# Performance work log

Measured on AMD Instinct MI355X. Metric: run time of the kernel, lower is better.

## Reference

```python
import jax, jax.numpy as jnp
import numpy as np

DIM = 1536
NH = 12
HD = DIM // NH          # 128
C = HD // 2             # 64 complex freq slots per head
DT = C - 2 * (C // 3)   # 22 temporal
DS = C // 3             # 21 per spatial axis
EPS = 1e-6
M_TAB = 64              # rope table length (>= max(f,h,w))


def _rope_tables():
    def tab(d):
        inv = 1.0 / (10000.0 ** (np.arange(d, dtype=np.float64) / d))
        ang = np.outer(np.arange(M_TAB, dtype=np.float64), inv)
        return np.cos(ang), np.sin(ang)
    ct, st = tab(DT)
    ch, sh = tab(DS)
    cw, sw = tab(DS)
    fc = np.concatenate([ct, ch, cw], axis=1).astype(np.float32)  # [M, 64]
    fs = np.concatenate([st, sh, sw], axis=1).astype(np.float32)
    return jnp.asarray(fc), jnp.asarray(fs)


def setup_inputs() -> dict:
    key = jax.random.key(0)
    ks = jax.random.split(key, 6)
    B, F, H, W = 1, 8, 22, 40
    L = F * H * W  # 7040
    s = 0.02
    x = jax.random.normal(ks[0], (B, L, DIM), jnp.float32)
    Wq = jax.random.normal(ks[1], (DIM, DIM), jnp.float32) * s
    Wk = jax.random.normal(ks[2], (DIM, DIM), jnp.float32) * s
    Wv = jax.random.normal(ks[3], (DIM, DIM), jnp.float32) * s
    Wo = jax.random.normal(ks[4], (DIM, DIM), jnp.float32) * s
    bk2 = jax.random.split(ks[5], 4)
    bq = jax.random.normal(bk2[0], (DIM,), jnp.float32) * s
    bk = jax.random.normal(bk2[1], (DIM,), jnp.float32) * s
    bv = jax.random.normal(bk2[2], (DIM,), jnp.float32) * s
    bo = jax.random.normal(bk2[3], (DIM,), jnp.float32) * s
    fc, fs = _rope_tables()
    return dict(x=x, Wq=Wq, bq=bq, Wk=Wk, bk=bk, Wv=Wv, bv=bv, Wo=Wo, bo=bo,
                gq=jnp.ones((DIM,), jnp.float32), gk=jnp.ones((DIM,), jnp.float32),
                freqs_cos=fc, freqs_sin=fs,
                num_frames=F, grid_h=H, grid_w=W,
                chunk_size=2, sink_size=1, max_attention_size=2640)


def _pos_table(tab, f, h, w):
    # tab: [M, 64] -> per-token [f*h*w, 64] via (t,h,w) axis split [22,21,21]
    t = jnp.broadcast_to(tab[:f, :DT][:, None, None, :], (f, h, w, DT))
    hh = jnp.broadcast_to(tab[:h, DT:DT + DS][None, :, None, :], (f, h, w, DS))
    ww = jnp.broadcast_to(tab[:w, DT + DS:][None, None, :, :], (f, h, w, DS))
    return jnp.concatenate([t, hh, ww], axis=-1).reshape(f * h * w, C)


def _forward(x, Wq, bq, Wk, bk, Wv, bv, Wo, bo, gq, gk, freqs_cos, freqs_sin,
             num_frames, grid_h, grid_w, chunk_size, sink_size, max_attention_size):
    B, L, D = x.shape
    lin = lambda t, W, b: jnp.einsum('bld,ed->ble', t, W) + b
    rms = lambda t, g: t * jax.lax.rsqrt(jnp.mean(t * t, axis=-1, keepdims=True) + EPS) * g

    q = rms(lin(x, Wq, bq), gq).reshape(B, L, NH, HD)
    k = rms(lin(x, Wk, bk), gk).reshape(B, L, NH, HD)
    v = lin(x, Wv, bv).reshape(B, L, NH, HD)

    # causal RoPE (start_frame=0)
    cosL = _pos_table(freqs_cos, num_frames, grid_h, grid_w)  # [L, 64]
    sinL = _pos_table(freqs_sin, num_frames, grid_h, grid_w)

    def rope(t):
        a = t.reshape(B, L, NH, C, 2)
        xr, xi = a[..., 0], a[..., 1]
        co = cosL[None, :, None, :]
        si = sinL[None, :, None, :]
        return jnp.stack([xr * co - xi * si, xr * si + xi * co], axis=-1).reshape(B, L, NH, HD)

    q = rope(q)
    k = rope(k)

    # loop attention, diffusion forcing: chunk i attends [0,(i+1)*block) with sink+window
    frame_seqlen = grid_h * grid_w
    block = frame_seqlen * chunk_size
    total_len = num_frames * frame_seqlen
    sink_end = sink_size * frame_seqlen
    num_chunks = -(-total_len // block)
    scale = 1.0 / (HD ** 0.5)

    def attn(qi, ki, vi):
        s = jnp.einsum('bqnd,bknd->bnqk', qi, ki) * scale
        p = jax.nn.softmax(s, axis=-1)
        return jnp.einsum('bnqk,bknd->bqnd', p, vi)

    outs = []
    for i in range(num_chunks):
        q_start = i * block
        q_end = min((i + 1) * block, total_len)
        qi = q[:, q_start:q_end]
        chunk_end = q_end
        if max_attention_size == -1 or sink_end == 0:
            if max_attention_size == -1:
                ki, vi = k[:, :chunk_end], v[:, :chunk_end]
            else:
                ws = max(0, chunk_end - max_attention_size)
                ki, vi = k[:, ws:chunk_end], v[:, ws:chunk_end]
        else:
            window = max_attention_size - sink_end
            ws = max(sink_end, chunk_end - window)
            ki = jnp.concatenate([k[:, :sink_end], k[:, ws:chunk_end]], axis=1)
            vi = jnp.concatenate([v[:, :sink_end], v[:, ws:chunk_end]], axis=1)
        outs.append(attn(qi, ki, vi))

    o = jnp.concatenate(outs, axis=1).reshape(B, L, D)
    return jnp.einsum('bld,ed->ble', o, Wo) + bo


def reference(x, Wq, bq, Wk, bk, Wv, bv, Wo, bo, gq, gk, freqs_cos, freqs_sin,
              num_frames, grid_h, grid_w, chunk_size, sink_size, max_attention_size):
    return _forward(x, Wq, bq, Wk, bk, Wv, bv, Wo, bo, gq, gk, freqs_cos, freqs_sin,
                    num_frames, grid_h, grid_w, chunk_size, sink_size, max_attention_size)
```

## Files before the change

### kernel.cpp

```cpp
#include <hip/hip_runtime.h>
#include <math.h>

typedef __attribute__((ext_vector_type(8))) short short8;
typedef __attribute__((ext_vector_type(4))) float f32x4;
typedef __attribute__((ext_vector_type(16))) float f32x16;
typedef __attribute__((ext_vector_type(4))) float f4;
typedef __attribute__((ext_vector_type(4))) unsigned short us4;
typedef __attribute__((ext_vector_type(2))) unsigned int u32x2;

#define MFMA16(a,b,c) __builtin_amdgcn_mfma_f32_16x16x32_bf16(a,b,c,0,0,0)
#define MFMA32(a,b,c) __builtin_amdgcn_mfma_f32_32x32x16_bf16(a,b,c,0,0,0)

__device__ __forceinline__ unsigned short f2bf(float f) {
  unsigned int u = __float_as_uint(f);
  u = (u + 0x7FFFu + ((u >> 16) & 1u)) >> 16;
  return (unsigned short)u;
}
__device__ __forceinline__ float bf2f(unsigned short b) {
  return __uint_as_float(((unsigned int)b) << 16);
}

typedef const __attribute__((address_space(1))) unsigned int* gas_t;
typedef __attribute__((address_space(3))) unsigned int* las_t;
__device__ __forceinline__ void gl16(const void* g, void* l) {
  __builtin_amdgcn_global_load_lds((gas_t)g, (las_t)l, 16, 0, 0);
}

__global__ void cvt_f32_bf16(const float* __restrict__ in,
                             unsigned short* __restrict__ out, int n4) {
  int i = blockIdx.x * blockDim.x + threadIdx.x;
  const int stride = gridDim.x * blockDim.x;
  for (; i < n4; i += stride) {
    f4 v = ((const f4*)in)[i];
    us4 o;
    o[0] = f2bf(v[0]); o[1] = f2bf(v[1]); o[2] = f2bf(v[2]); o[3] = f2bf(v[3]);
    ((us4*)out)[i] = o;
  }
}

template<int F32OUT>
__global__ __launch_bounds__(256)
void gemm_bt(const unsigned short* __restrict__ A,
             const unsigned short* __restrict__ B,
             const float* __restrict__ bias,
             unsigned short* __restrict__ obf,
             float* __restrict__ of32,
             int K, int ldo)
{
  const int tid = threadIdx.x;
  const int wave = tid >> 6, lane = tid & 63, lg = lane >> 4, lr = lane & 15;
  const int wr = wave >> 1, wc = wave & 1;
  const int m0 = blockIdx.y * 128, n0 = blockIdx.x * 128;

  __shared__ __align__(16) unsigned short Al[128 * 32];
  __shared__ __align__(16) unsigned short Bl[128 * 32];

  f32x4 acc[4][4];
#pragma unroll
  for (int m = 0; m < 4; ++m)
#pragma unroll
    for (int n = 0; n < 4; ++n) acc[m][n] = (f32x4){0.f, 0.f, 0.f, 0.f};

  const int r0 = tid >> 2, r1 = (tid + 256) >> 2;
  const int c0 = (tid & 3) * 8;
  const long arow0 = (long)(m0 + r0) * K, arow1 = (long)(m0 + r1) * K;
  const long brow0 = (long)(n0 + r0) * K, brow1 = (long)(n0 + r1) * K;

  for (int k0 = 0; k0 < K; k0 += 32) {
    gl16(A + arow0 + k0 + c0, (char*)Al + tid * 16);
    gl16(A + arow1 + k0 + c0, (char*)Al + (tid + 256) * 16);
    gl16(B + brow0 + k0 + c0, (char*)Bl + tid * 16);
    gl16(B + brow1 + k0 + c0, (char*)Bl + (tid + 256) * 16);
    __syncthreads();
    short8 af[4], bf[4];
#pragma unroll
    for (int m = 0; m < 4; ++m)
      af[m] = *(const short8*)(Al + (wr * 64 + m * 16 + lr) * 32 + lg * 8);
#pragma unroll
    for (int n = 0; n < 4; ++n)
      bf[n] = *(const short8*)(Bl + (wc * 64 + n * 16 + lr) * 32 + lg * 8);
#pragma unroll
    for (int m = 0; m < 4; ++m)
#pragma unroll
      for (int n = 0; n < 4; ++n)
        acc[m][n] = MFMA16(af[m], bf[n], acc[m][n]);
    __syncthreads();
  }

#pragma unroll
  for (int n = 0; n < 4; ++n) {
    const int col = n0 + wc * 64 + n * 16 + lr;
    const float bs = bias[col];
#pragma unroll
    for (int m = 0; m < 4; ++m) {
      const int row = m0 + wr * 64 + m * 16 + lg * 4;
#pragma unroll
      for (int r = 0; r < 4; ++r) {
        float v = acc[m][n][r] + bs;
        if (F32OUT) of32[(long)(row + r) * ldo + col] = v;
        else        obf[(long)(row + r) * ldo + col] = f2bf(v);
      }
    }
  }
}

__global__ __launch_bounds__(256)
void normrope(unsigned short* __restrict__ qkv, const float* __restrict__ g,
              const float* __restrict__ fc, const float* __restrict__ fs,
              int colOff, float oscale)
{
  const int l = blockIdx.x, tid = threadIdx.x;
  __shared__ float rowbuf[1536];
  __shared__ float sred[4];
  unsigned short* rp = qkv + (long)l * 4608 + colOff;

  float ss = 0.f;
  if (tid < 192) {
    short8 v = *(const short8*)(rp + tid * 8);
#pragma unroll
    for (int e = 0; e < 8; ++e) {
      float f = bf2f((unsigned short)v[e]);
      rowbuf[tid * 8 + e] = f;
      ss += f * f;
    }
  }
#pragma unroll
  for (int m = 32; m; m >>= 1) ss += __shfl_xor(ss, m, 64);
  if ((tid & 63) == 0) sred[tid >> 6] = ss;
  __syncthreads();
  const float rs = rsqrtf((sred[0] + sred[1] + sred[2] + sred[3]) * (1.f / 1536.f) + 1e-6f);

  const int f_ = l / 880, rem = l % 880, h_ = rem / 40, w_ = rem % 40;
#pragma unroll
  for (int j = 0; j < 3; ++j) {
    int p = tid + j * 256;
    int head = p >> 6, c = p & 63;
    int e = head * 128 + 2 * c;
    int tr = (c < 22) ? f_ : ((c < 43) ? h_ : w_);
    float co = fc[tr * 64 + c], si = fs[tr * 64 + c];
    float xr = rowbuf[e] * rs * g[e];
    float xi = rowbuf[e + 1] * rs * g[e + 1];
    float yr = (xr * co - xi * si) * oscale;
    float yi = (xr * si + xi * co) * oscale;
    unsigned int pk = (unsigned int)f2bf(yr) | ((unsigned int)f2bf(yi) << 16);
    *(unsigned int*)(rp + e) = pk;
  }
}

__device__ __forceinline__ void issueK(const unsigned short* __restrict__ qkv,
                                       int h, int t, int kvlen, int woff, int tid,
                                       unsigned short* Kbuf)
{
#pragma unroll
  for (int i = 0; i < 4; ++i) {
    int s = i * 256 + tid;
    int kvl = s >> 4;
    int dc = (s & 15) ^ (kvl & 7);
    int j = t * 64 + kvl; j = j < kvlen ? j : kvlen - 1;
    int gk = j + (j >= 880 ? woff : 0);
    gl16(qkv + (long)gk * 4608 + 1536 + h * 128 + dc * 8, (char*)Kbuf + s * 16);
  }
}

__device__ __forceinline__ void loadV(const unsigned short* __restrict__ qkv,
                                      int h, int t, int kvlen, int woff, int tid,
                                      short8 vp[2][2])
{
#pragma unroll
  for (int i = 0; i < 2; ++i) {
    int task = i * 256 + tid;
    int dc = task & 15, kp = task >> 4;
    int kvl = kp * 2;
    int j0 = t * 64 + kvl, j1 = j0 + 1;
    j0 = j0 < kvlen ? j0 : kvlen - 1;
    j1 = j1 < kvlen ? j1 : kvlen - 1;
    int g0 = j0 + (j0 >= 880 ? woff : 0);
    int g1 = j1 + (j1 >= 880 ? woff : 0);
    vp[i][0] = *(const short8*)(qkv + (long)g0 * 4608 + 3072 + h * 128 + dc * 8);
    vp[i][1] = *(const short8*)(qkv + (long)g1 * 4608 + 3072 + h * 128 + dc * 8);
  }
}

__device__ __forceinline__ void writeV(int tid, short8 vp[2][2], unsigned short* Vt)
{
#pragma unroll
  for (int i = 0; i < 2; ++i) {
    int task = i * 256 + tid;
    int dc = task & 15, kp = task >> 4;
    int kvl = kp * 2;
#pragma unroll
    for (int e = 0; e < 8; ++e) {
      int d = dc * 8 + e;
      int byte = d * 128 + kvl * 2;
      byte ^= (((d & 7) ^ ((d >> 3) & 7)) << 4);
      *(unsigned int*)((char*)Vt + byte) =
          (unsigned int)(unsigned short)vp[i][0][e] |
          ((unsigned int)(unsigned short)vp[i][1][e] << 16);
    }
  }
}

__global__ __launch_bounds__(256, 2)
void attn_kern(const unsigned short* __restrict__ qkv,
               unsigned short* __restrict__ ob)
{
  const int qt = blockIdx.x, ci = blockIdx.y, h = blockIdx.z;
  const int tid = threadIdx.x, wave = tid >> 6, lane = tid & 63;
  const int l31 = lane & 31, hh = lane >> 5;
  const int chunk_start = ci * 1760, chunk_end = chunk_start + 1760;
  const int wstart = (ci == 0) ? 880 : ci * 1760;
  const int woff = wstart - 880;
  const int kvlen = 880 + (chunk_end - wstart);
  const int q0 = chunk_start + qt * 128;

  __shared__ __align__(16) unsigned short Kl[2][64 * 128];
  __shared__ __align__(16) unsigned short Vt[128 * 64];

  int qr = q0 + wave * 32 + l31;
  if (qr >= chunk_end) qr = chunk_end - 1;
  const unsigned short* qp = qkv + (long)qr * 4608 + h * 128;
  short8 qf[8];
#pragma unroll
  for (int st = 0; st < 8; ++st) qf[st] = *(const short8*)(qp + st * 16 + hh * 8);

  f32x16 Oc[4];
#pragma unroll
  for (int i = 0; i < 4; ++i)
#pragma unroll
    for (int j = 0; j < 16; ++j) Oc[i][j] = 0.f;
  float m_run = -1e30f, l_run = 0.f;

  const int nt = (kvlen + 63) >> 6;
  short8 vp[2][2];
  issueK(qkv, h, 0, kvlen, woff, tid, &Kl[0][0]);
  loadV(qkv, h, 0, kvlen, woff, tid, vp);
  writeV(tid, vp, Vt);
  __syncthreads();

  for (int t = 0; t < nt; ++t) {
    const int cur = t & 1;
    const bool pf = (t + 1 < nt);
    if (pf) {
      issueK(qkv, h, t + 1, kvlen, woff, tid, &Kl[cur ^ 1][0]);
      loadV(qkv, h, t + 1, kvlen, woff, tid, vp);
    }

    f32x16 s0, s1;
#pragma unroll
    for (int j = 0; j < 16; ++j) { s0[j] = 0.f; s1[j] = 0.f; }
    __builtin_amdgcn_s_setprio(1);
#pragma unroll
    for (int st = 0; st < 8; ++st) {
      int off = 32 * st + 16 * hh;
      int b0 = l31 * 256 + (off ^ ((l31 & 7) << 4));
      short8 k0 = *(const short8*)((const char*)&Kl[cur][0] + b0);
      s0 = MFMA32(k0, qf[st], s0);
      int b1 = (32 + l31) * 256 + (off ^ ((l31 & 7) << 4));
      short8 k1 = *(const short8*)((const char*)&Kl[cur][0] + b1);
      s1 = MFMA32(k1, qf[st], s1);
    }
    __builtin_amdgcn_s_setprio(0);

    if (t * 64 + 64 > kvlen) {
#pragma unroll
      for (int r = 0; r < 16; ++r) {
        int kv0 = t * 64 + (r & 3) + 8 * (r >> 2) + 4 * hh;
        if (kv0 >= kvlen)      s0[r] = -1e30f;
        if (kv0 + 32 >= kvlen) s1[r] = -1e30f;
      }
    }

    float pm = s0[0];
#pragma unroll
    for (int r = 1; r < 16; ++r) pm = fmaxf(pm, s0[r]);
#pragma unroll
    for (int r = 0; r < 16; ++r) pm = fmaxf(pm, s1[r]);
    pm = fmaxf(pm, __shfl_xor(pm, 32, 64));
    float mn = fmaxf(m_run, pm);
    float al = __builtin_amdgcn_exp2f(m_run - mn);
    float sum = 0.f;
#pragma unroll
    for (int r = 0; r < 16; ++r) {
      s0[r] = __builtin_amdgcn_exp2f(s0[r] - mn); sum += s0[r];
      s1[r] = __builtin_amdgcn_exp2f(s1[r] - mn); sum += s1[r];
    }
    sum += __shfl_xor(sum, 32, 64);
    l_run = l_run * al + sum;
    m_run = mn;

    unsigned int w0[8], w1[8];
#pragma unroll
    for (int m = 0; m < 8; ++m) {
      w0[m] = (unsigned int)f2bf(s0[2 * m]) | ((unsigned int)f2bf(s0[2 * m + 1]) << 16);
      w1[m] = (unsigned int)f2bf(s1[2 * m]) | ((unsigned int)f2bf(s1[2 * m + 1]) << 16);
    }

#pragma unroll
    for (int i = 0; i < 4; ++i)
#pragma unroll
      for (int j = 0; j < 16; ++j) Oc[i][j] *= al;

    __builtin_amdgcn_s_setprio(1);
#pragma unroll
    for (int s = 0; s < 4; ++s) {
      const unsigned int* w = (s < 2) ? w0 : w1;
      const int lo4 = (s & 1) * 4;
      unsigned int x0 = __shfl_xor(w[lo4 + 2], 32, 64);
      unsigned int x1 = __shfl_xor(w[lo4 + 3], 32, 64);
      unsigned int y0 = __shfl_xor(w[lo4],     32, 64);
      unsigned int y1 = __shfl_xor(w[lo4 + 1], 32, 64);
      unsigned int fw[4];
      fw[0] = hh ? x0 : w[lo4];
      fw[1] = hh ? x1 : w[lo4 + 1];
      fw[2] = hh ? w[lo4 + 2] : y0;
      fw[3] = hh ? w[lo4 + 3] : y1;
      short8 pb;
#pragma unroll
      for (int m = 0; m < 4; ++m) {
        pb[2 * m]     = (short)(fw[m] & 0xFFFF);
        pb[2 * m + 1] = (short)(fw[m] >> 16);
      }
#pragma unroll
      for (int dt = 0; dt < 4; ++dt) {
        int d = dt * 32 + l31;
        int byte = d * 128 + s * 32 + hh * 16;
        byte ^= (((d & 7) ^ ((d >> 3) & 7)) << 4);
        short8 vf = *(const short8*)((const char*)Vt + byte);
        Oc[dt] = MFMA32(vf, pb, Oc[dt]);
      }
    }
    __builtin_amdgcn_s_setprio(0);

    __syncthreads();
    if (pf) writeV(tid, vp, Vt);
    __syncthreads();
  }

  const int qg = q0 + wave * 32 + l31;
  if (qg < chunk_end) {
    const float inv = 1.f / l_run;
    unsigned short* op = ob + (long)qg * 1536 + h * 128;
#pragma unroll
    for (int dt = 0; dt < 4; ++dt) {
#pragma unroll
      for (int gblk = 0; gblk < 4; ++gblk) {
        int d = dt * 32 + gblk * 8 + hh * 4;
        unsigned int u0 = (unsigned int)f2bf(Oc[dt][4 * gblk]     * inv) |
                          ((unsigned int)f2bf(Oc[dt][4 * gblk + 1] * inv) << 16);
        unsigned int u1 = (unsigned int)f2bf(Oc[dt][4 * gblk + 2] * inv) |
                          ((unsigned int)f2bf(Oc[dt][4 * gblk + 3] * inv) << 16);
        u32x2 uu; uu[0] = u0; uu[1] = u1;
        *(u32x2*)(op + d) = uu;
      }
    }
  }
}

extern "C" void kernel_launch(void* const* d_in, const int* in_sizes, int n_in,
                              void* d_out, int out_size, void* d_ws, size_t ws_size,
                              hipStream_t stream)
{
  const float* x  = (const float*)d_in[0];
  const float* Wq = (const float*)d_in[1];
  const float* bq = (const float*)d_in[2];
  const float* Wk = (const float*)d_in[3];
  const float* bk = (const float*)d_in[4];
  const float* Wv = (const float*)d_in[5];
  const float* bv = (const float*)d_in[6];
  const float* Wo = (const float*)d_in[7];
  const float* bo = (const float*)d_in[8];
  const float* gq = (const float*)d_in[9];
  const float* gk = (const float*)d_in[10];
  const float* fc = (const float*)d_in[11];
  const float* fs = (const float*)d_in[12];

  char* ws = (char*)d_ws;
  unsigned short* xb   = (unsigned short*)(ws);
  unsigned short* wcat = (unsigned short*)(ws + 21626880);
  unsigned short* wob  = (unsigned short*)(ws + 35782656);
  float*          bcat = (float*)(ws + 40501248);
  unsigned short* qkv  = (unsigned short*)(ws + 40519680);
  unsigned short* obuf = (unsigned short*)(ws + 105400320);

  cvt_f32_bf16<<<2048, 256, 0, stream>>>(x,  xb,   10813440 / 4);
  cvt_f32_bf16<<<1024, 256, 0, stream>>>(Wq, wcat,            2359296 / 4);
  cvt_f32_bf16<<<1024, 256, 0, stream>>>(Wk, wcat + 2359296,  2359296 / 4);
  cvt_f32_bf16<<<1024, 256, 0, stream>>>(Wv, wcat + 4718592,  2359296 / 4);
  cvt_f32_bf16<<<1024, 256, 0, stream>>>(Wo, wob,             2359296 / 4);
  hipMemcpyAsync(bcat,        bq, 1536 * 4, hipMemcpyDeviceToDevice, stream);
  hipMemcpyAsync(bcat + 1536, bk, 1536 * 4, hipMemcpyDeviceToDevice, stream);
  hipMemcpyAsync(bcat + 3072, bv, 1536 * 4, hipMemcpyDeviceToDevice, stream);

  gemm_bt<0><<<dim3(36, 55), 256, 0, stream>>>(xb, wcat, bcat, qkv, nullptr, 1536, 4608);

  const float qsc = (float)(1.4426950408889634 / sqrt(128.0));
  normrope<<<7040, 256, 0, stream>>>(qkv, gq, fc, fs, 0,    qsc);
  normrope<<<7040, 256, 0, stream>>>(qkv, gk, fc, fs, 1536, 1.0f);

  attn_kern<<<dim3(14, 4, 12), 256, 0, stream>>>(qkv, obuf);

  gemm_bt<1><<<dim3(12, 55), 256, 0, stream>>>(obuf, wob, bo, nullptr, (float*)d_out, 1536, 1536);
}
```

Baseline: 476.1 us.

## Double-buffer V tile, defer softmax rescale, and use cheaper bf16 packing

The attention kernel now keeps two V tiles in LDS, so the next tile is written before the PV MMAs and one barrier per iteration is dropped. It also skips the online-softmax rescale of the output accumulators when no lane's running max rises by more than 8 (in log2 units). Max and sum use tree reductions, and the bf16 packing uses round-half-up plus a byte-permute instead of round-to-nearest-even. In exchange, LDS use per block grows by 16 KB, which could hurt occupancy. Deferred rescaling and the changed rounding alter numerics slightly.

After: 449.2 us. 1.06x faster.

```diff
diff --git a/kernel.cpp b/kernel.cpp
--- a/kernel.cpp
+++ b/kernel.cpp
@@ -18,6 +18,11 @@
 }
 __device__ __forceinline__ float bf2f(unsigned short b) {
   return __uint_as_float(((unsigned int)b) << 16);
+}
+__device__ __forceinline__ unsigned int pk2(float a, float b) {
+  unsigned int au = __float_as_uint(a) + 0x8000u;
+  unsigned int bu = __float_as_uint(b) + 0x8000u;
+  return __builtin_amdgcn_perm(bu, au, 0x07060302u);
 }
 
 typedef const __attribute__((address_space(1))) unsigned int* gas_t;
@@ -214,7 +219,7 @@
   const int q0 = chunk_start + qt * 128;
 
   __shared__ __align__(16) unsigned short Kl[2][64 * 128];
-  __shared__ __align__(16) unsigned short Vt[128 * 64];
+  __shared__ __align__(16) unsigned short Vt[2][128 * 64];
 
   int qr = q0 + wave * 32 + l31;
   if (qr >= chunk_end) qr = chunk_end - 1;
@@ -234,7 +239,7 @@
   short8 vp[2][2];
   issueK(qkv, h, 0, kvlen, woff, tid, &Kl[0][0]);
   loadV(qkv, h, 0, kvlen, woff, tid, vp);
-  writeV(tid, vp, Vt);
+  writeV(tid, vp, &Vt[0][0]);
   __syncthreads();
 
   for (int t = 0; t < nt; ++t) {
@@ -270,35 +275,52 @@
       }
     }
 
-    float pm = s0[0];
-#pragma unroll
-    for (int r = 1; r < 16; ++r) pm = fmaxf(pm, s0[r]);
-#pragma unroll
-    for (int r = 0; r < 16; ++r) pm = fmaxf(pm, s1[r]);
-    pm = fmaxf(pm, __shfl_xor(pm, 32, 64));
-    float mn = fmaxf(m_run, pm);
-    float al = __builtin_amdgcn_exp2f(m_run - mn);
-    float sum = 0.f;
+    float mx[16];
+#pragma unroll
+    for (int r = 0; r < 16; ++r) mx[r] = fmaxf(s0[r], s1[r]);
+#pragma unroll
+    for (int w = 8; w; w >>= 1)
+#pragma unroll
+      for (int r = 0; r < w; ++r) mx[r] = fmaxf(mx[r], mx[r + w]);
+    float pm = fmaxf(mx[0], __shfl_xor(mx[0], 32, 64));
+
+    const bool defer = __all(pm <= m_run + 8.f);
+    const float mn = defer ? m_run : fmaxf(m_run, pm);
+
 #pragma unroll
     for (int r = 0; r < 16; ++r) {
-      s0[r] = __builtin_amdgcn_exp2f(s0[r] - mn); sum += s0[r];
-      s1[r] = __builtin_amdgcn_exp2f(s1[r] - mn); sum += s1[r];
-    }
-    sum += __shfl_xor(sum, 32, 64);
-    l_run = l_run * al + sum;
-    m_run = mn;
+      s0[r] = __builtin_amdgcn_exp2f(s0[r] - mn);
+      s1[r] = __builtin_amdgcn_exp2f(s1[r] - mn);
+    }
+    float sm[16];
+#pragma unroll
+    for (int r = 0; r < 16; ++r) sm[r] = s0[r] + s1[r];
+#pragma unroll
+    for (int w = 8; w; w >>= 1)
+#pragma unroll
+      for (int r = 0; r < w; ++r) sm[r] += sm[r + w];
+    float sum = sm[0] + __shfl_xor(sm[0], 32, 64);
+
+    if (defer) {
+      l_run += sum;
+    } else {
+      float al = __builtin_amdgcn_exp2f(m_run - mn);
+      l_run = l_run * al + sum;
+      m_run = mn;
+#pragma unroll
+      for (int i = 0; i < 4; ++i)
+#pragma unroll
+        for (int j = 0; j < 16; ++j) Oc[i][j] *= al;
+    }
 
     unsigned int w0[8], w1[8];
 #pragma unroll
     for (int m = 0; m < 8; ++m) {
-      w0[m] = (unsigned int)f2bf(s0[2 * m]) | ((unsigned int)f2bf(s0[2 * m + 1]) << 16);
-      w1[m] = (unsigned int)f2bf(s1[2 * m]) | ((unsigned int)f2bf(s1[2 * m + 1]) << 16);
-    }
-
-#pragma unroll
-    for (int i = 0; i < 4; ++i)
-#pragma unroll
-      for (int j = 0; j < 16; ++j) Oc[i][j] *= al;
+      w0[m] = pk2(s0[2 * m], s0[2 * m + 1]);
+      w1[m] = pk2(s1[2 * m], s1[2 * m + 1]);
+    }
+
+    if (pf) writeV(tid, vp, &Vt[cur ^ 1][0]);
 
     __builtin_amdgcn_s_setprio(1);
 #pragma unroll
@@ -314,25 +336,18 @@
       fw[1] = hh ? x1 : w[lo4 + 1];
       fw[2] = hh ? w[lo4 + 2] : y0;
       fw[3] = hh ? w[lo4 + 3] : y1;
-      short8 pb;
-#pragma unroll
-      for (int m = 0; m < 4; ++m) {
-        pb[2 * m]     = (short)(fw[m] & 0xFFFF);
-        pb[2 * m + 1] = (short)(fw[m] >> 16);
-      }
+      short8 pb = *(const short8*)fw;
 #pragma unroll
       for (int dt = 0; dt < 4; ++dt) {
         int d = dt * 32 + l31;
         int byte = d * 128 + s * 32 + hh * 16;
         byte ^= (((d & 7) ^ ((d >> 3) & 7)) << 4);
-        short8 vf = *(const short8*)((const char*)Vt + byte);
+        short8 vf = *(const short8*)((const char*)&Vt[cur][0] + byte);
         Oc[dt] = MFMA32(vf, pb, Oc[dt]);
       }
     }
     __builtin_amdgcn_s_setprio(0);
 
-    __syncthreads();
-    if (pf) writeV(tid, vp, Vt);
     __syncthreads();
   }
 
@@ -345,10 +360,8 @@
 #pragma unroll
       for (int gblk = 0; gblk < 4; ++gblk) {
         int d = dt * 32 + gblk * 8 + hh * 4;
-        unsigned int u0 = (unsigned int)f2bf(Oc[dt][4 * gblk]     * inv) |
-                          ((unsigned int)f2bf(Oc[dt][4 * gblk + 1] * inv) << 16);
-        unsigned int u1 = (unsigned int)f2bf(Oc[dt][4 * gblk + 2] * inv) |
-                          ((unsigned int)f2bf(Oc[dt][4 * gblk + 3] * inv) << 16);
+        unsigned int u0 = pk2(Oc[dt][4 * gblk]     * inv, Oc[dt][4 * gblk + 1] * inv);
+        unsigned int u1 = pk2(Oc[dt][4 * gblk + 2] * inv, Oc[dt][4 * gblk + 3] * inv);
         u32x2 uu; uu[0] = u0; uu[1] = u1;
         *(u32x2*)(op + d) = uu;
       }
```
